# Performance work log

Measured on AMD Instinct MI355X. Metric: run time of the kernel, lower is better.

## Reference

```python
import jax, jax.numpy as jnp
import numpy as np


def setup_inputs() -> dict:
    key = jax.random.key(0)
    k1, k2, k3 = jax.random.split(key, 3)
    B, N = 4096, 8192
    output = jax.random.normal(k1, (B, N), dtype=jnp.float32)
    mean_grad = jax.random.normal(k2, (N,), dtype=jnp.float32)
    var_grad = jax.random.uniform(k3, (N,), dtype=jnp.float32)
    return {"output": output, "mean_grad": mean_grad, "var_grad": var_grad, "k": 4}


def reference(output, mean_grad, var_grad, k):
    # nan_checker: zero out NaN/Inf entries
    out = jnp.where(jnp.isnan(output) | jnp.isinf(output), jnp.zeros((), output.dtype), output)
    # circular finite difference: Conv1d kernel [-1, 1, 0] with circular 'same' padding
    # y[b, i] = out[b, i] - out[b, (i-1) mod N]
    grad_Y = out - jnp.roll(out, 1, axis=1)
    std = jnp.sqrt(var_grad)
    lower = mean_grad - k * std  # [N], broadcast over batch
    upper = mean_grad + k * std
    mask = (grad_Y < lower) | (grad_Y > upper)
    return jnp.where(mask, jnp.zeros((), out.dtype), out)
```

## Files before the change

kernel.cpp:

```cpp
#include <hip/hip_runtime.h>
#include <hip/hip_bf16.h>


typedef float f32x4 __attribute__((ext_vector_type(4)));

__device__ __forceinline__ float sanitize(float x) {
    unsigned u = __float_as_uint(x);
    return ((u & 0x7f800000u) == 0x7f800000u) ? 0.0f : x;
}

__global__ __launch_bounds__(256) void correction_kernel(
    const float* __restrict__ in,
    const float* __restrict__ mean_grad,
    const float* __restrict__ var_grad,
    const int* __restrict__ kptr,
    float* __restrict__ y,
    int N)
{
    const int row = blockIdx.x;
    const float kf = (float)(*kptr);
    const float* __restrict__ rp = in + (size_t)row * (size_t)N;
    float* __restrict__ ro = y + (size_t)row * (size_t)N;
    const int vec_per_row = N >> 2;

    for (int v = threadIdx.x; v < vec_per_row; v += blockDim.x) {
        const int i = v << 2;
        f32x4 x = *reinterpret_cast<const f32x4*>(rp + i);
        float prev = rp[(i == 0) ? (N - 1) : (i - 1)];

        float s0 = sanitize(x.x);
        float s1 = sanitize(x.y);
        float s2 = sanitize(x.z);
        float s3 = sanitize(x.w);
        float sp = sanitize(prev);

        f32x4 m  = *reinterpret_cast<const f32x4*>(mean_grad + i);
        f32x4 vr = *reinterpret_cast<const f32x4*>(var_grad + i);

        float t0 = kf * sqrtf(vr.x);
        float t1 = kf * sqrtf(vr.y);
        float t2 = kf * sqrtf(vr.z);
        float t3 = kf * sqrtf(vr.w);

        float d0 = s0 - sp;
        float d1 = s1 - s0;
        float d2 = s2 - s1;
        float d3 = s3 - s2;

        f32x4 r;
        r.x = (d0 < m.x - t0 || d0 > m.x + t0) ? 0.0f : s0;
        r.y = (d1 < m.y - t1 || d1 > m.y + t1) ? 0.0f : s1;
        r.z = (d2 < m.z - t2 || d2 > m.z + t2) ? 0.0f : s2;
        r.w = (d3 < m.w - t3 || d3 > m.w + t3) ? 0.0f : s3;

        __builtin_nontemporal_store(r, reinterpret_cast<f32x4*>(ro + i));
    }
}

extern "C" void kernel_launch(void* const* d_in, const int* in_sizes, int n_in,
                              void* d_out, int out_size, void* d_ws, size_t ws_size,
                              hipStream_t stream) {
    const float* in        = (const float*)d_in[0];
    const float* mean_grad = (const float*)d_in[1];
    const float* var_grad  = (const float*)d_in[2];
    const int*   kptr      = (const int*)d_in[3];
    float* y = (float*)d_out;

    const int N = in_sizes[1];
    const int B = in_sizes[0] / N;

    dim3 grid(B);
    dim3 block(256);
    correction_kernel<<<grid, block, 0, stream>>>(in, mean_grad, var_grad, kptr, y, N);
}
```

Baseline: 44.82 us.

## Tile rows per block, hoist per-column bounds, use wave shuffle for neighbor

Changes the grid from one block per row to 2D tiles: each block handles a 1024-column strip across 16 rows, so the mean/var loads, sqrt and bound computations happen once per thread and are reused across rows. The previous-element load is replaced by a cross-lane shuffle, with only lane 0 of each wave doing a scalar load. This cuts redundant parameter traffic and ALU work, but shrinks the grid and assumes N divisible by 1024 and B divisible by 16.

```diff
diff --git a/kernel.cpp b/kernel.cpp
--- a/kernel.cpp
+++ b/kernel.cpp
@@ -9,51 +9,59 @@
     return ((u & 0x7f800000u) == 0x7f800000u) ? 0.0f : x;
 }
 
-__global__ __launch_bounds__(256) void correction_kernel(
+#define RPB 16
+#define TPB 256
+
+__global__ __launch_bounds__(TPB) void correction_kernel(
     const float* __restrict__ in,
     const float* __restrict__ mean_grad,
     const float* __restrict__ var_grad,
     const int* __restrict__ kptr,
     float* __restrict__ y,
-    int N)
+    int N, int colTiles)
 {
-    const int row = blockIdx.x;
+    const int ct = blockIdx.x % colTiles;
+    const int rt = blockIdx.x / colTiles;
+    const int c  = ct * (TPB * 4) + threadIdx.x * 4;
+    const int lane = threadIdx.x & 63;
+    const int pc = (c == 0) ? (N - 1) : (c - 1);
     const float kf = (float)(*kptr);
-    const float* __restrict__ rp = in + (size_t)row * (size_t)N;
-    float* __restrict__ ro = y + (size_t)row * (size_t)N;
-    const int vec_per_row = N >> 2;
 
-    for (int v = threadIdx.x; v < vec_per_row; v += blockDim.x) {
-        const int i = v << 2;
-        f32x4 x = *reinterpret_cast<const f32x4*>(rp + i);
-        float prev = rp[(i == 0) ? (N - 1) : (i - 1)];
+    f32x4 m  = *reinterpret_cast<const f32x4*>(mean_grad + c);
+    f32x4 vr = *reinterpret_cast<const f32x4*>(var_grad + c);
+    f32x4 lo, hi;
+    lo.x = m.x - kf * sqrtf(vr.x);  hi.x = m.x + kf * sqrtf(vr.x);
+    lo.y = m.y - kf * sqrtf(vr.y);  hi.y = m.y + kf * sqrtf(vr.y);
+    lo.z = m.z - kf * sqrtf(vr.z);  hi.z = m.z + kf * sqrtf(vr.z);
+    lo.w = m.w - kf * sqrtf(vr.w);  hi.w = m.w + kf * sqrtf(vr.w);
+
+    const int r0 = rt * RPB;
+    #pragma unroll 4
+    for (int r = r0; r < r0 + RPB; ++r) {
+        const float* __restrict__ rp = in + (size_t)r * (size_t)N;
+        f32x4 x = *reinterpret_cast<const f32x4*>(rp + c);
 
         float s0 = sanitize(x.x);
         float s1 = sanitize(x.y);
         float s2 = sanitize(x.z);
         float s3 = sanitize(x.w);
-        float sp = sanitize(prev);
 
-        f32x4 m  = *reinterpret_cast<const f32x4*>(mean_grad + i);
-        f32x4 vr = *reinterpret_cast<const f32x4*>(var_grad + i);
-
-        float t0 = kf * sqrtf(vr.x);
-        float t1 = kf * sqrtf(vr.y);
-        float t2 = kf * sqrtf(vr.z);
-        float t3 = kf * sqrtf(vr.w);
+        float sp = __shfl_up(s3, 1);
+        if (lane == 0) sp = sanitize(rp[pc]);
 
         float d0 = s0 - sp;
         float d1 = s1 - s0;
         float d2 = s2 - s1;
         float d3 = s3 - s2;
 
-        f32x4 r;
-        r.x = (d0 < m.x - t0 || d0 > m.x + t0) ? 0.0f : s0;
-        r.y = (d1 < m.y - t1 || d1 > m.y + t1) ? 0.0f : s1;
-        r.z = (d2 < m.z - t2 || d2 > m.z + t2) ? 0.0f : s2;
-        r.w = (d3 < m.w - t3 || d3 > m.w + t3) ? 0.0f : s3;
+        f32x4 out;
+        out.x = (d0 < lo.x || d0 > hi.x) ? 0.0f : s0;
+        out.y = (d1 < lo.y || d1 > hi.y) ? 0.0f : s1;
+        out.z = (d2 < lo.z || d2 > hi.z) ? 0.0f : s2;
+        out.w = (d3 < lo.w || d3 > hi.w) ? 0.0f : s3;
 
-        __builtin_nontemporal_store(r, reinterpret_cast<f32x4*>(ro + i));
+        __builtin_nontemporal_store(out,
+            reinterpret_cast<f32x4*>(y + (size_t)r * (size_t)N + c));
     }
 }
 
@@ -69,7 +77,9 @@
     const int N = in_sizes[1];
     const int B = in_sizes[0] / N;
 
-    dim3 grid(B);
-    dim3 block(256);
-    correction_kernel<<<grid, block, 0, stream>>>(in, mean_grad, var_grad, kptr, y, N);
+    const int colTiles = N / (TPB * 4);
+    const int rowTiles = B / RPB;
+    dim3 grid(colTiles * rowTiles);
+    dim3 block(TPB);
+    correction_kernel<<<grid, block, 0, stream>>>(in, mean_grad, var_grad, kptr, y, N, colTiles);
 }
```

Result: slower. 46.53 us (+3.8%).
